# Performance work log

Hardware: AMD Instinct MI355X
Metric: run time of the kernel (lower is better)

Reference implementation:

```python
import jax, jax.numpy as jnp
import numpy as np

L, B, D, H = 2048, 2, 1024, 16


def setup_inputs() -> dict:
    key = jax.random.key(0)
    ks = jax.random.split(key, 4)
    x = jax.random.normal(ks[0], (L, B, D), dtype=jnp.float32)
    W_in = jax.random.normal(ks[1], (3 * D, D), dtype=jnp.float32) * (1.0 / np.sqrt(D))
    b_in = jnp.zeros((3 * D,), dtype=jnp.float32)
    W_out = jax.random.normal(ks[2], (D, D), dtype=jnp.float32) * (1.0 / np.sqrt(D))
    b_out = jnp.zeros((D,), dtype=jnp.float32)
    mask = jnp.zeros((1, L, L), dtype=jnp.float32)
    return {"q": x, "k": x, "v": x, "mask": mask,
            "W_in": W_in, "b_in": b_in, "W_out": W_out, "b_out": b_out,
            "num_heads": H}


def reference(q, k, v, mask, W_in, b_in, W_out, b_out, num_heads):
    l, b, d = q.shape
    hd = d // num_heads
    # fused QKV projection (q == k == v in this module)
    qkv = q @ W_in.T + b_in                      # (l, b, 3d)
    qh, kh, vh = jnp.split(qkv, 3, axis=-1)      # each (l, b, d)

    def to_heads(t):
        # (l, b, d) -> (b*h, l, hd)
        return t.reshape(l, b * num_heads, hd).transpose(1, 0, 2)

    qh, kh, vh = to_heads(qh), to_heads(kh), to_heads(vh)
    qh = qh / jnp.sqrt(jnp.asarray(hd, dtype=qh.dtype))
    scores = jnp.einsum('nld,nmd->nlm', qh, kh) + mask   # (b*h, l, l)
    attn = jax.nn.softmax(scores, axis=-1)
    z = jnp.einsum('nlm,nmd->nld', attn, vh)             # (b*h, l, hd)
    z = z.transpose(1, 0, 2).reshape(l * b, d)
    z = z @ W_out.T + b_out
    return z.reshape(l, b, d)
```

## Files before the change

kernel.cpp:

```cpp
#include <hip/hip_runtime.h>


typedef short  s8v  __attribute__((ext_vector_type(8)));
typedef short  s4vv __attribute__((ext_vector_type(4)));
typedef float  f4v  __attribute__((ext_vector_type(4)));
typedef float  f4l  __attribute__((ext_vector_type(4)));
typedef float  f16v __attribute__((ext_vector_type(16)));
typedef int    i4v  __attribute__((ext_vector_type(4)));
typedef int    i2v  __attribute__((ext_vector_type(2)));

__device__ __forceinline__ short f2bf(float f) {
  union { float f; unsigned u; } x; x.f = f;
  unsigned r = (x.u + 0x7fffu + ((x.u >> 16) & 1u)) >> 16;
  return (short)r;
}

__device__ __forceinline__ int cvtpk(float lo, float hi) {
  int r;
  asm("v_cvt_pk_bf16_f32 %0, %1, %2" : "=v"(r) : "v"(lo), "v"(hi));
  return r;
}

#define GLDS16(gp, lp) __builtin_amdgcn_global_load_lds( \
    (const __attribute__((address_space(1))) void*)(gp),  \
    (__attribute__((address_space(3))) void*)(lp), 16, 0, 0)

#define LOG2E 1.4426950408889634f

__global__ __launch_bounds__(256) void prep(const float* __restrict__ x,
                                            const float* __restrict__ wi,
                                            const float* __restrict__ wo,
                                            const float* __restrict__ mask,
                                            short* __restrict__ xb,
                                            short* __restrict__ wib,
                                            short* __restrict__ wob,
                                            unsigned* __restrict__ flags) {
  const int b = blockIdx.x;
  if (b < 8192) {
    int i = b * 256 + threadIdx.x;
    const float* src; short* dst; int off;
    if (i < 1048576)               { src = x;  dst = xb;  off = i; }
    else if (i < 1048576 + 786432) { src = wi; dst = wib; off = i - 1048576; }
    else                           { src = wo; dst = wob; off = i - 1835008; }
    f4l v = ((const f4l*)src)[off];
    s4vv o;
    o[0] = f2bf(v[0]); o[1] = f2bf(v[1]); o[2] = f2bf(v[2]); o[3] = f2bf(v[3]);
    ((s4vv*)dst)[off] = o;
  } else {
    const int l = b - 8192;
    const int qt = l >> 7;
    const int t = threadIdx.x;
    const float* row = mask + ((size_t)l << 11) + (t << 3);
    f4l a = *(const f4l*)row;
    f4l bb = *(const f4l*)(row + 4);
    bool nz = (a[0] != 0.f) | (a[1] != 0.f) | (a[2] != 0.f) | (a[3] != 0.f) |
              (bb[0] != 0.f) | (bb[1] != 0.f) | (bb[2] != 0.f) | (bb[3] != 0.f);
    unsigned long long bal = __ballot(nz);
    const int w = t >> 6, lane = t & 63;
    if (lane == 0 && bal) {
      unsigned bits = 0;
#pragma unroll
      for (int g = 0; g < 8; ++g)
        if ((bal >> (g << 3)) & 0xFFull) bits |= 1u << ((w << 3) + g);
      atomicOr(&flags[qt], bits);
    }
  }
}

__global__ __launch_bounds__(512, 1) void gemm_qkv(const short* __restrict__ A,
                                                   const short* __restrict__ B,
                                                   const float* __restrict__ bin,
                                                   short* __restrict__ Qh,
                                                   short* __restrict__ Kh,
                                                   short* __restrict__ VT) {
  __shared__ __align__(16) short As[2][16384];
  __shared__ __align__(16) short Bs[2][16384];
  const int tid = threadIdx.x;
  const int w = tid >> 6, lane = tid & 63;
  const int g = lane >> 4, c15 = lane & 15;
  const int wr = w >> 2, wc = w & 3;
  const int bx = blockIdx.x;
  const int by = blockIdx.y;
  const int rowbase = by << 8;
  const int colbase = bx << 8;
  const int rl = lane >> 3, sp = lane & 7;
  const int swz = (sp ^ rl) << 3;

  f4v acc[8][4] = {};

#define VMW(N) asm volatile("s_waitcnt vmcnt(" #N ")" ::: "memory")
#define BAR()  do { __builtin_amdgcn_s_barrier(); asm volatile("" ::: "memory"); } while (0)

#define STAGE(bi, t) do {                                                        \
    _Pragma("unroll")                                                            \
    for (int c = 0; c < 4; ++c) {                                                \
      const int chunk = (w << 2) + c;                                 \
      const int row = (chunk << 3) + rl;                             \
      GLDS16(A + ((size_t)(rowbase + row) << 10) + ((t) << 6) + swz,             \
             &As[bi][chunk << 9]);                                               \
      GLDS16(B + ((size_t)(colbase + row) << 10) + ((t) << 6) + swz,             \
             &Bs[bi][chunk << 9]);                                               \
    } } while (0)

  STAGE(0, 0);

#pragma unroll 1
  for (int t = 0; t < 16; ++t) {
    if (t < 15) { STAGE((t + 1) & 1, t + 1); VMW(8); }
    else        { VMW(0); }
    BAR();
    const char* Ac = (const char*)&As[t & 1][0];
    const char* Bc = (const char*)&Bs[t & 1][0];
#pragma unroll
    for (int kk = 0; kk < 2; ++kk) {
      s8v af[8], bf[4];
#pragma unroll
      for (int m = 0; m < 8; ++m) {
        const int row = (wr << 7) + (m << 4) + c15;
        af[m] = *(const s8v*)(Ac + row * 128 + ((((kk << 2) | g) ^ (row & 7)) << 4));
      }
#pragma unroll
      for (int nn = 0; nn < 4; ++nn) {
        const int col = (wc << 6) + (nn << 4) + c15;
        bf[nn] = *(const s8v*)(Bc + col * 128 + ((((kk << 2) | g) ^ (col & 7)) << 4));
      }
#pragma unroll
      for (int m = 0; m < 8; ++m)
#pragma unroll
        for (int nn = 0; nn < 4; ++nn)
          acc[m][nn] = __builtin_amdgcn_mfma_f32_16x16x32_bf16(af[m], bf[nn], acc[m][nn], 0, 0, 0);
    }
    BAR();
  }
#undef STAGE
#undef VMW
#undef BAR

  const int r0 = rowbase + (wr << 7) + (g << 2);
  const int c0 = colbase + (wc << 6) + c15;
  const int which = colbase >> 10;
#pragma unroll
  for (int nn = 0; nn < 4; ++nn) {
    const int col = c0 + (nn << 4);
    const int dd = col & 1023;
    const int hh = dd >> 6, ee = dd & 63;
    const float bias = bin[col];
    if (which == 2) {
      unsigned* v0p = (unsigned*)(VT + ((((size_t)hh << 6) + ee) << 11));
      unsigned* v1p = (unsigned*)(VT + (((((size_t)hh + 16) << 6) + ee) << 11));
#pragma unroll
      for (int m = 0; m < 8; ++m) {
        const int li0 = (r0 >> 1) + (m << 3);
        v0p[li0 >> 1] = (unsigned)cvtpk(acc[m][nn][0] + bias, acc[m][nn][2] + bias);
        v1p[li0 >> 1] = (unsigned)cvtpk(acc[m][nn][1] + bias, acc[m][nn][3] + bias);
      }
    } else {
      const float mul = (which == 0) ? 0.125f * LOG2E : 1.0f;
      short* dst = (which == 0) ? Qh : Kh;
#pragma unroll
      for (int m = 0; m < 8; ++m) {
#pragma unroll
        for (int j = 0; j < 4; ++j) {
          const int row = r0 + (m << 4) + j;
          const int li = row >> 1, bb = row & 1;
          const int nh = (bb << 4) + hh;
          dst[(((size_t)nh * 2048 + li) << 6) + ee] = f2bf((acc[m][nn][j] + bias) * mul);
        }
      }
    }
  }
}

__global__ __launch_bounds__(256) void gemm_out(const short* __restrict__ A,
                                                const short* __restrict__ B,
                                                const float* __restrict__ bout,
                                                float* __restrict__ out) {
  __shared__ __align__(16) short As[128 * 64];
  __shared__ __align__(16) short Bs[64 * 64];
  const int tid = threadIdx.x;
  const int w = tid >> 6, lane = tid & 63;
  const int g = lane >> 4, c15 = lane & 15;
  const int orig = blockIdx.x;
  const int xcd = orig & 7, j6 = orig >> 3;
  const int colblk = (xcd << 1) + (j6 & 1);
  const int rowblk = j6 >> 1;
  const int rowbase = rowblk << 7;
  const int colbase = colblk << 6;
  const int rl = lane >> 3, sp = lane & 7;
  const int swz = (sp ^ rl) << 3;

  f4v acc[2][4] = {};

  for (int kt = 0; kt < 16; ++kt) {
#pragma unroll
    for (int c2 = 0; c2 < 4; ++c2) {
      const int chunk = (w << 2) + c2;
      const int row = (chunk << 3) + rl;
      GLDS16(A + ((size_t)(rowbase + row) << 10) + (kt << 6) + swz, &As[chunk << 9]);
    }
#pragma unroll
    for (int c2 = 0; c2 < 2; ++c2) {
      const int chunk = (w << 1) + c2;
      const int row = (chunk << 3) + rl;
      GLDS16(B + ((size_t)(colbase + row) << 10) + (kt << 6) + swz, &Bs[chunk << 9]);
    }
    __syncthreads();
#pragma unroll
    for (int kk = 0; kk < 2; ++kk) {
      s8v af[2], bf[4];
#pragma unroll
      for (int m = 0; m < 2; ++m) {
        const int row = (w << 5) + (m << 4) + c15;
        af[m] = *(const s8v*)((const char*)As + row * 128 + ((((kk << 2) | g) ^ (row & 7)) << 4));
      }
#pragma unroll
      for (int nn = 0; nn < 4; ++nn) {
        const int col = (nn << 4) + c15;
        bf[nn] = *(const s8v*)((const char*)Bs + col * 128 + ((((kk << 2) | g) ^ (col & 7)) << 4));
      }
#pragma unroll
      for (int m = 0; m < 2; ++m)
#pragma unroll
        for (int nn = 0; nn < 4; ++nn)
          acc[m][nn] = __builtin_amdgcn_mfma_f32_16x16x32_bf16(af[m], bf[nn], acc[m][nn], 0, 0, 0);
    }
    __syncthreads();
  }

  const int r0 = rowbase + (w << 5) + (g << 2);
  const int c0 = colbase + c15;
#pragma unroll
  for (int nn = 0; nn < 4; ++nn) {
    const int col = c0 + (nn << 4);
    const float bias = bout[col];
#pragma unroll
    for (int m = 0; m < 2; ++m) {
#pragma unroll
      for (int j = 0; j < 4; ++j) {
        const int row = r0 + (m << 4) + j;
        out[((size_t)row << 10) + col] = acc[m][nn][j] + bias;
      }
    }
  }
}

__global__ __launch_bounds__(256, 2) void attn(const short* __restrict__ Qh,
                                               const short* __restrict__ Kh,
                                               const short* __restrict__ VTg,
                                               const float* __restrict__ mask,
                                               const unsigned* __restrict__ mflags,
                                               short* __restrict__ Z) {
  __shared__ __align__(16) short Ks[2][128 * 64];
  __shared__ __align__(16) short Vs[2][64 * 128];
  const int tid = threadIdx.x;
  const int w = tid >> 6, lane = tid & 63;
  const int q5 = lane & 31, hi = lane >> 5;
  const int orig = blockIdx.x;
  const int wg = ((orig & 7) << 6) + (orig >> 3);
  const int n = wg >> 4, qt = wg & 15;
  const int krow8 = lane >> 3;
  const int ssw = ((lane & 7) ^ krow8) << 3;
  const int vrow = lane >> 4, vslot = lane & 15;

  const int qg = (qt << 7) + (w << 5) + q5;

  const short* Qp = Qh + (((size_t)n * 2048 + qg) << 6);
  s8v bq[4];
#pragma unroll
  for (int ks = 0; ks < 4; ++ks)
    bq[ks] = *(const s8v*)(Qp + (ks << 4) + (hi << 3));

  const short* Kbase = Kh + ((size_t)n << 17);
  const short* Vbase = VTg + ((size_t)n << 17);
  const float* mrow = mask + ((size_t)qg << 11) + (hi << 2);
  const unsigned mbits = mflags[qt];
  const int kslot = q5 & 7;
  const int vsl15 = q5 & 15;

  f16v oA0, oA1, zz;
#pragma unroll
  for (int e = 0; e < 16; ++e) { oA0[e] = 0.0f; oA1[e] = 0.0f; zz[e] = 0.0f; }
  float ls0 = 0.0f, ls1 = 0.0f;
  f16v sS[4];

#define STAGEK(bi, t) do {                                                      \
    _Pragma("unroll")                                                           \
    for (int c = 0; c < 4; ++c) {                                               \
      const int chunk = (w << 2) + c;                                           \
      GLDS16(Kbase + ((size_t)(((t) << 7) + (chunk << 3) + krow8) << 6) + ssw,  \
             &Ks[bi][chunk << 9]);                                              \
    } } while (0)
#define STAGEV(bi, t) do {                                                      \
    _Pragma("unroll")                                                           \
    for (int c = 0; c < 4; ++c) {                                               \
      const int chunk = (w << 2) + c;                                           \
      const int r = (chunk << 2) + vrow;                                        \
      GLDS16(Vbase + ((size_t)r << 11) + ((t) << 7) + ((vslot ^ (r & 15)) << 3),\
             &Vs[bi][chunk << 9]);                                              \
    } } while (0)

#define QKM(bi) do {                                                            \
    const char* Kc = (const char*)&Ks[bi][0];                                   \
    __builtin_amdgcn_s_setprio(1);                                              \
    _Pragma("unroll")                                                           \
    for (int ks = 0; ks < 4; ++ks) {                                            \
      const int so = ((2 * ks + hi) ^ kslot) << 4;                              \
      s8v a0 = *(const s8v*)(Kc + q5 * 128 + so);                               \
      s8v a1 = *(const s8v*)(Kc + (q5 + 32) * 128 + so);                        \
      s8v a2 = *(const s8v*)(Kc + (q5 + 64) * 128 + so);                        \
      s8v a3 = *(const s8v*)(Kc + (q5 + 96) * 128 + so);                        \
      if (ks == 0) {                                                            \
        sS[0] = __builtin_amdgcn_mfma_f32_32x32x16_bf16(a0, bq[0], zz, 0, 0, 0);\
        sS[1] = __builtin_amdgcn_mfma_f32_32x32x16_bf16(a1, bq[0], zz, 0, 0, 0);\
        sS[2] = __builtin_amdgcn_mfma_f32_32x32x16_bf16(a2, bq[0], zz, 0, 0, 0);\
        sS[3] = __builtin_amdgcn_mfma_f32_32x32x16_bf16(a3, bq[0], zz, 0, 0, 0);\
      } else {                                                                  \
        sS[0] = __builtin_amdgcn_mfma_f32_32x32x16_bf16(a0, bq[ks], sS[0], 0,0,0);\
        sS[1] = __builtin_amdgcn_mfma_f32_32x32x16_bf16(a1, bq[ks], sS[1], 0,0,0);\
        sS[2] = __builtin_amdgcn_mfma_f32_32x32x16_bf16(a2, bq[ks], sS[2], 0,0,0);\
        sS[3] = __builtin_amdgcn_mfma_f32_32x32x16_bf16(a3, bq[ks], sS[3], 0,0,0);\
      } }                                                                       \
    __builtin_amdgcn_s_setprio(0); } while (0)

#define SMPV(t, bi) do {                                                        \
    if ((mbits >> ((t) << 1)) & 1u) {                                           \
      const float* mp = mrow + ((t) << 7);                                      \
      _Pragma("unroll")                                                         \
      for (int c = 0; c < 4; ++c) {                                             \
        f4l m0 = *(const f4l*)(mp + (c << 3));                                  \
        f4l m1 = *(const f4l*)(mp + 32 + (c << 3));                             \
        _Pragma("unroll")                                                       \
        for (int jj = 0; jj < 4; ++jj) {                                        \
          sS[0][(c << 2) + jj] += m0[jj] * LOG2E;                               \
          sS[1][(c << 2) + jj] += m1[jj] * LOG2E;                               \
        } } }                                                                   \
    if ((mbits >> (((t) << 1) + 1)) & 1u) {                                     \
      const float* mp = mrow + ((t) << 7) + 64;                                 \
      _Pragma("unroll")                                                         \
      for (int c = 0; c < 4; ++c) {                                             \
        f4l m0 = *(const f4l*)(mp + (c << 3));                                  \
        f4l m1 = *(const f4l*)(mp + 32 + (c << 3));                             \
        _Pragma("unroll")                                                       \
        for (int jj = 0; jj < 4; ++jj) {                                        \
          sS[2][(c << 2) + jj] += m0[jj] * LOG2E;                               \
          sS[3][(c << 2) + jj] += m1[jj] * LOG2E;                               \
        } } }                                                                   \
    _Pragma("unroll")                                                           \
    for (int r = 0; r < 16; ++r) {                                              \
      float a = __builtin_amdgcn_exp2f(sS[0][r]); sS[0][r] = a; ls0 += a;       \
      float b = __builtin_amdgcn_exp2f(sS[1][r]); sS[1][r] = b; ls1 += b;       \
      float c = __builtin_amdgcn_exp2f(sS[2][r]); sS[2][r] = c; ls0 += c;       \
      float d = __builtin_amdgcn_exp2f(sS[3][r]); sS[3][r] = d; ls1 += d;       \
    }                                                                           \
    const char* Vc = (const char*)&Vs[bi][0];                                   \
    __builtin_amdgcn_s_setprio(1);                                              \
    _Pragma("unroll")                                                           \
    for (int kb = 0; kb < 4; ++kb) {                                            \
      _Pragma("unroll")                                                         \
      for (int ks2 = 0; ks2 < 2; ++ks2) {                                       \
        const int ro = ks2 << 3;                                                \
        int P0 = cvtpk(sS[kb][ro + 0], sS[kb][ro + 1]);                         \
        int P1 = cvtpk(sS[kb][ro + 2], sS[kb][ro + 3]);                         \
        int P2 = cvtpk(sS[kb][ro + 4], sS[kb][ro + 5]);                         \
        int P3 = cvtpk(sS[kb][ro + 6], sS[kb][ro + 7]);                         \
        int x0 = __shfl_xor(P2, 32);                                            \
        int x1 = __shfl_xor(P3, 32);                                            \
        int x2 = __shfl_xor(P0, 32);                                            \
        int x3 = __shfl_xor(P1, 32);                                            \
        union { i4v i; s8v s; } pu;                                             \
        pu.i[0] = hi ? x0 : P0;                                                 \
        pu.i[1] = hi ? x1 : P1;                                                 \
        pu.i[2] = hi ? P2 : x2;                                                 \
        pu.i[3] = hi ? P3 : x3;                                                 \
        const int p = (kb << 1) + ks2;                                          \
        const int so = (((p << 1) + hi) ^ vsl15) << 4;                          \
        s8v av0 = *(const s8v*)(Vc + q5 * 256 + so);                            \
        s8v av1 = *(const s8v*)(Vc + (q5 + 32) * 256 + so);                     \
        oA0 = __builtin_amdgcn_mfma_f32_32x32x16_bf16(av0, pu.s, oA0, 0, 0, 0); \
        oA1 = __builtin_amdgcn_mfma_f32_32x32x16_bf16(av1, pu.s, oA1, 0, 0, 0); \
      } }                                                                       \
    __builtin_amdgcn_s_setprio(0); } while (0)

  STAGEK(0, 0); STAGEV(0, 0);
  __syncthreads();

  for (int t = 0; t < 15; ++t) {
    STAGEK((t + 1) & 1, t + 1);
    STAGEV((t + 1) & 1, t + 1);
    QKM(t & 1);
    SMPV(t, t & 1);
    __syncthreads();
  }
  QKM(1);
  SMPV(15, 1);

#undef STAGEK
#undef STAGEV
#undef QKM
#undef SMPV

  float lrun = ls0 + ls1;
  lrun += __shfl_xor(lrun, 32);
  const float invl = 1.0f / lrun;
  short* zp = Z + ((((size_t)qg << 1) + (n >> 4)) << 10) + ((n & 15) << 6);
#pragma unroll
  for (int c = 0; c < 4; ++c) {
    const int d0 = (c << 3) + (hi << 2);
    i2v w0, w1;
    w0[0] = cvtpk(oA0[(c << 2) + 0] * invl, oA0[(c << 2) + 1] * invl);
    w0[1] = cvtpk(oA0[(c << 2) + 2] * invl, oA0[(c << 2) + 3] * invl);
    *(i2v*)(zp + d0) = w0;
    w1[0] = cvtpk(oA1[(c << 2) + 0] * invl, oA1[(c << 2) + 1] * invl);
    w1[1] = cvtpk(oA1[(c << 2) + 2] * invl, oA1[(c << 2) + 3] * invl);
    *(i2v*)(zp + 32 + d0) = w1;
  }
}

extern "C" void kernel_launch(void* const* d_in, const int* in_sizes, int n_in,
                              void* d_out, int out_size, void* d_ws, size_t ws_size,
                              hipStream_t stream) {
  const float* xq   = (const float*)d_in[0];
  const float* mask = (const float*)d_in[3];
  const float* Win  = (const float*)d_in[4];
  const float* bin  = (const float*)d_in[5];
  const float* Wout = (const float*)d_in[6];
  const float* bout = (const float*)d_in[7];
  float* out = (float*)d_out;

  char* ws = (char*)d_ws;
  short* xb  = (short*)(ws);
  short* wib = (short*)(ws + (8ull  << 20));
  short* wob = (short*)(ws + (14ull << 20));
  short* Qh  = (short*)(ws + (16ull << 20));
  short* Kh  = (short*)(ws + (24ull << 20));
  short* VTg = (short*)(ws + (32ull << 20));
  short* Zb  = (short*)(ws + (40ull << 20));
  unsigned* mflags = (unsigned*)(ws + (48ull << 20));

  hipMemsetAsync(mflags, 0, 16 * sizeof(unsigned), stream);
  prep<<<8192 + 2048, 256, 0, stream>>>(xq, Win, Wout, mask, xb, wib, wob, mflags);
  gemm_qkv<<<dim3(12, 16), 512, 0, stream>>>(xb, wib, bin, Qh, Kh, VTg);
  attn<<<512, 256, 0, stream>>>(Qh, Kh, VTg, mask, mflags, Zb);
  gemm_out<<<512, 256, 0, stream>>>(Zb, wob, bout, out);
}
```

Before: 127.7 us.

## Software-pipeline QK^T one tile ahead of softmax-PV with double score registers

Restructures the attention main loop so that the QK^T MFMAs for tile t+1 are issued alongside the softmax and PV work for tile t, using two score register sets (sSA/sSB) and a loop unrolled by two. K is staged one tile further ahead than V so the K tile for the next QK is resident when it is needed. This is meant to overlap matrix-core work with exp/convert/shuffle work and hide the dependency chain between the score MFMAs and the softmax. In exchange it doubles the score accumulator registers (64 more VGPRs), which may lower occupancy or cause spills.

```diff
diff --git a/kernel.cpp b/kernel.cpp
--- a/kernel.cpp
+++ b/kernel.cpp
@@ -94,8 +94,8 @@
 #define STAGE(bi, t) do {                                                        \
     _Pragma("unroll")                                                            \
     for (int c = 0; c < 4; ++c) {                                                \
-      const int chunk = (w << 2) + c;                                 \
-      const int row = (chunk << 3) + rl;                             \
+      const int chunk = (w << 2) + c;                                            \
+      const int row = (chunk << 3) + rl;                                         \
       GLDS16(A + ((size_t)(rowbase + row) << 10) + ((t) << 6) + swz,             \
              &As[bi][chunk << 9]);                                               \
       GLDS16(B + ((size_t)(colbase + row) << 10) + ((t) << 6) + swz,             \
@@ -281,7 +281,7 @@
 #pragma unroll
   for (int e = 0; e < 16; ++e) { oA0[e] = 0.0f; oA1[e] = 0.0f; zz[e] = 0.0f; }
   float ls0 = 0.0f, ls1 = 0.0f;
-  f16v sS[4];
+  f16v sSA[4], sSB[4];
 
 #define STAGEK(bi, t) do {                                                      \
     _Pragma("unroll")                                                           \
@@ -299,7 +299,7 @@
              &Vs[bi][chunk << 9]);                                              \
     } } while (0)
 
-#define QKM(bi) do {                                                            \
+#define QKM(SS, bi) do {                                                        \
     const char* Kc = (const char*)&Ks[bi][0];                                   \
     __builtin_amdgcn_s_setprio(1);                                              \
     _Pragma("unroll")                                                           \
@@ -310,19 +310,19 @@
       s8v a2 = *(const s8v*)(Kc + (q5 + 64) * 128 + so);                        \
       s8v a3 = *(const s8v*)(Kc + (q5 + 96) * 128 + so);                        \
       if (ks == 0) {                                                            \
-        sS[0] = __builtin_amdgcn_mfma_f32_32x32x16_bf16(a0, bq[0], zz, 0, 0, 0);\
-        sS[1] = __builtin_amdgcn_mfma_f32_32x32x16_bf16(a1, bq[0], zz, 0, 0, 0);\
-        sS[2] = __builtin_amdgcn_mfma_f32_32x32x16_bf16(a2, bq[0], zz, 0, 0, 0);\
-        sS[3] = __builtin_amdgcn_mfma_f32_32x32x16_bf16(a3, bq[0], zz, 0, 0, 0);\
+        SS[0] = __builtin_amdgcn_mfma_f32_32x32x16_bf16(a0, bq[0], zz, 0, 0, 0);\
+        SS[1] = __builtin_amdgcn_mfma_f32_32x32x16_bf16(a1, bq[0], zz, 0, 0, 0);\
+        SS[2] = __builtin_amdgcn_mfma_f32_32x32x16_bf16(a2, bq[0], zz, 0, 0, 0);\
+        SS[3] = __builtin_amdgcn_mfma_f32_32x32x16_bf16(a3, bq[0], zz, 0, 0, 0);\
       } else {                                                                  \
-        sS[0] = __builtin_amdgcn_mfma_f32_32x32x16_bf16(a0, bq[ks], sS[0], 0,0,0);\
-        sS[1] = __builtin_amdgcn_mfma_f32_32x32x16_bf16(a1, bq[ks], sS[1], 0,0,0);\
-        sS[2] = __builtin_amdgcn_mfma_f32_32x32x16_bf16(a2, bq[ks], sS[2], 0,0,0);\
-        sS[3] = __builtin_amdgcn_mfma_f32_32x32x16_bf16(a3, bq[ks], sS[3], 0,0,0);\
+        SS[0] = __builtin_amdgcn_mfma_f32_32x32x16_bf16(a0, bq[ks], SS[0], 0,0,0);\
+        SS[1] = __builtin_amdgcn_mfma_f32_32x32x16_bf16(a1, bq[ks], SS[1], 0,0,0);\
+        SS[2] = __builtin_amdgcn_mfma_f32_32x32x16_bf16(a2, bq[ks], SS[2], 0,0,0);\
+        SS[3] = __builtin_amdgcn_mfma_f32_32x32x16_bf16(a3, bq[ks], SS[3], 0,0,0);\
       } }                                                                       \
     __builtin_amdgcn_s_setprio(0); } while (0)
 
-#define SMPV(t, bi) do {                                                        \
+#define SMPV(SS, t, bi) do {                                                    \
     if ((mbits >> ((t) << 1)) & 1u) {                                           \
       const float* mp = mrow + ((t) << 7);                                      \
       _Pragma("unroll")                                                         \
@@ -331,8 +331,8 @@
         f4l m1 = *(const f4l*)(mp + 32 + (c << 3));                             \
         _Pragma("unroll")                                                       \
         for (int jj = 0; jj < 4; ++jj) {                                        \
-          sS[0][(c << 2) + jj] += m0[jj] * LOG2E;                               \
-          sS[1][(c << 2) + jj] += m1[jj] * LOG2E;                               \
+          SS[0][(c << 2) + jj] += m0[jj] * LOG2E;                               \
+          SS[1][(c << 2) + jj] += m1[jj] * LOG2E;                               \
         } } }                                                                   \
     if ((mbits >> (((t) << 1) + 1)) & 1u) {                                     \
       const float* mp = mrow + ((t) << 7) + 64;                                 \
@@ -342,15 +342,15 @@
         f4l m1 = *(const f4l*)(mp + 32 + (c << 3));                             \
         _Pragma("unroll")                                                       \
         for (int jj = 0; jj < 4; ++jj) {                                        \
-          sS[2][(c << 2) + jj] += m0[jj] * LOG2E;                               \
-          sS[3][(c << 2) + jj] += m1[jj] * LOG2E;                               \
+          SS[2][(c << 2) + jj] += m0[jj] * LOG2E;                               \
+          SS[3][(c << 2) + jj] += m1[jj] * LOG2E;                               \
         } } }                                                                   \
     _Pragma("unroll")                                                           \
     for (int r = 0; r < 16; ++r) {                                              \
-      float a = __builtin_amdgcn_exp2f(sS[0][r]); sS[0][r] = a; ls0 += a;       \
-      float b = __builtin_amdgcn_exp2f(sS[1][r]); sS[1][r] = b; ls1 += b;       \
-      float c = __builtin_amdgcn_exp2f(sS[2][r]); sS[2][r] = c; ls0 += c;       \
-      float d = __builtin_amdgcn_exp2f(sS[3][r]); sS[3][r] = d; ls1 += d;       \
+      float a = __builtin_amdgcn_exp2f(SS[0][r]); SS[0][r] = a; ls0 += a;       \
+      float b = __builtin_amdgcn_exp2f(SS[1][r]); SS[1][r] = b; ls1 += b;       \
+      float c = __builtin_amdgcn_exp2f(SS[2][r]); SS[2][r] = c; ls0 += c;       \
+      float d = __builtin_amdgcn_exp2f(SS[3][r]); SS[3][r] = d; ls1 += d;       \
     }                                                                           \
     const char* Vc = (const char*)&Vs[bi][0];                                   \
     __builtin_amdgcn_s_setprio(1);                                              \
@@ -359,10 +359,10 @@
       _Pragma("unroll")                                                         \
       for (int ks2 = 0; ks2 < 2; ++ks2) {                                       \
         const int ro = ks2 << 3;                                                \
-        int P0 = cvtpk(sS[kb][ro + 0], sS[kb][ro + 1]);                         \
-        int P1 = cvtpk(sS[kb][ro + 2], sS[kb][ro + 3]);                         \
-        int P2 = cvtpk(sS[kb][ro + 4], sS[kb][ro + 5]);                         \
-        int P3 = cvtpk(sS[kb][ro + 6], sS[kb][ro + 7]);                         \
+        int P0 = cvtpk(SS[kb][ro + 0], SS[kb][ro + 1]);                         \
+        int P1 = cvtpk(SS[kb][ro + 2], SS[kb][ro + 3]);                         \
+        int P2 = cvtpk(SS[kb][ro + 4], SS[kb][ro + 5]);                         \
+        int P3 = cvtpk(SS[kb][ro + 6], SS[kb][ro + 7]);                         \
         int x0 = __shfl_xor(P2, 32);                                            \
         int x1 = __shfl_xor(P3, 32);                                            \
         int x2 = __shfl_xor(P0, 32);                                            \
@@ -381,18 +381,30 @@
       } }                                                                       \
     __builtin_amdgcn_s_setprio(0); } while (0)
 
-  STAGEK(0, 0); STAGEV(0, 0);
+  STAGEK(0, 0); STAGEV(0, 0); STAGEK(1, 1);
   __syncthreads();
-
-  for (int t = 0; t < 15; ++t) {
-    STAGEK((t + 1) & 1, t + 1);
-    STAGEV((t + 1) & 1, t + 1);
-    QKM(t & 1);
-    SMPV(t, t & 1);
+  QKM(sSA, 0);
+  __syncthreads();
+
+#pragma unroll 1
+  for (int tt = 0; tt < 7; ++tt) {
+    const int t = tt << 1;
+    STAGEV(1, t + 1);
+    STAGEK(0, t + 2);
+    QKM(sSB, 1);
+    SMPV(sSA, t, 0);
     __syncthreads();
-  }
-  QKM(1);
-  SMPV(15, 1);
+    STAGEV(0, t + 2);
+    STAGEK(1, t + 3);
+    QKM(sSA, 0);
+    SMPV(sSB, t + 1, 1);
+    __syncthreads();
+  }
+  STAGEV(1, 15);
+  QKM(sSB, 1);
+  SMPV(sSA, 14, 0);
+  __syncthreads();
+  SMPV(sSB, 15, 1);
 
 #undef STAGEK
 #undef STAGEV
```

New measurement: 196.0 us. +53.5%, slower.
